# Performance work log

Measured on AMD Instinct MI355X. Metric: run time of the kernel, lower is better.

Reference implementation:

```python
import jax, jax.numpy as jnp
import numpy as np

B, N, C, H, D = 1, 4096, 256, 8, 64  # batch, seq, channels, heads, head_dim


def setup_inputs() -> dict:
    key = jax.random.key(0)
    ks = jax.random.split(key, 11)
    s = 0.02
    return {
        "q_x": jax.random.normal(ks[0], (B, N, C), jnp.float32),
        "k_x": jax.random.normal(ks[1], (B, N, C), jnp.float32),
        "v_x": jax.random.normal(ks[2], (B, N, C), jnp.float32),
        "bias": jax.random.normal(ks[3], (B, 1, N, N), jnp.float32),
        "wq": jax.random.normal(ks[4], (H * D, C), jnp.float32) * s,
        "wk": jax.random.normal(ks[5], (H * D, C), jnp.float32) * s,
        "wv": jax.random.normal(ks[6], (H * D, C), jnp.float32) * s,
        "wg": jax.random.normal(ks[7], (H * D, C), jnp.float32) * s,
        "bg": jnp.ones((H * D,), jnp.float32),  # gating bias init = 1
        "wo": jax.random.normal(ks[8], (C, H * D), jnp.float32) * s,
        "bo": jnp.zeros((C,), jnp.float32),
        "q_chunk_size": 256,
        "kv_chunk_size": 1024,
    }


def reference(q_x, k_x, v_x, bias, wq, wk, wv, wg, bg, wo, bo,
              q_chunk_size, kv_chunk_size):
    # The chunked Rabe-Staats loop computes exact softmax attention; the
    # chunk sizes are memory knobs only, so the reference computes the
    # mathematically identical full attention.
    q = (q_x @ wq.T).reshape(*q_x.shape[:-1], H, D) / jnp.sqrt(jnp.asarray(D, q_x.dtype))
    k = (k_x @ wk.T).reshape(*k_x.shape[:-1], H, D)
    v = (v_x @ wv.T).reshape(*v_x.shape[:-1], H, D)
    logits = jnp.einsum("bqhd,bkhd->bhqk", q, k) + bias  # [B,H,Q,K]
    p = jax.nn.softmax(logits, axis=-1)
    o = jnp.einsum("bkhd,bhqk->bqhd", v, p)  # [B,Q,H,D]
    g = jax.nn.sigmoid(q_x @ wg.T + bg).reshape(*q_x.shape[:-1], H, D)
    o = o * g
    o = o.reshape(*o.shape[:-2], H * D)
    return o @ wo.T + bo
```

## Files before the change

kernel.cpp:

```cpp
#include <hip/hip_runtime.h>
#include <stdint.h>

#define NN 4096
#define CC 256
#define HD 512
#define DD 64
#define KSPLIT 3

typedef __attribute__((ext_vector_type(8))) short short8;
typedef __attribute__((ext_vector_type(4))) float floatx4;

__device__ __forceinline__ unsigned short f2bf(float x) {
    union { float f; unsigned int u; } v; v.f = x;
    unsigned int u = v.u + 0x7fffu + ((v.u >> 16) & 1u);
    return (unsigned short)(u >> 16);
}
__device__ __forceinline__ float bf2f(unsigned short s) {
    union { unsigned int u; float f; } v; v.u = ((unsigned int)s) << 16;
    return v.f;
}

#if defined(__has_builtin) && __has_builtin(__builtin_amdgcn_cvt_pk_bf16_f32)
typedef __attribute__((ext_vector_type(2))) __bf16 bf16x2_t;
__device__ __forceinline__ unsigned int pack2bf(float a, float b) {
    union { bf16x2_t v; unsigned int u; } x;
    x.v = __builtin_amdgcn_cvt_pk_bf16_f32(a, b);
    return x.u;
}
#else
__device__ __forceinline__ unsigned int pack2bf(float a, float b) {
    return ((unsigned int)f2bf(b) << 16) | (unsigned int)f2bf(a);
}
#endif

#define GLOAD_LDS(gp, lp) __builtin_amdgcn_global_load_lds(                    \
    (__attribute__((address_space(1))) void*)(gp),                             \
    (__attribute__((address_space(3))) void*)(lp), 16, 0, 0)

__global__ __launch_bounds__(256) void prep_kernel(
    const float* __restrict__ qx, const float* __restrict__ kx,
    const float* __restrict__ vx,
    const float* __restrict__ wq, const float* __restrict__ wk,
    const float* __restrict__ wv, const float* __restrict__ wg,
    const float* __restrict__ wo,
    unsigned short* __restrict__ qxb, unsigned short* __restrict__ kxb,
    unsigned short* __restrict__ vxb, unsigned short* __restrict__ Wb,
    unsigned short* __restrict__ wob)
{
    const int z = blockIdx.y;
    const float* src; unsigned short* dst; int n; float s = 1.0f;
    switch (z) {
        case 0: src = qx; dst = qxb; n = NN * CC; break;
        case 1: src = kx; dst = kxb; n = NN * CC; break;
        case 2: src = vx; dst = vxb; n = NN * CC; break;
        case 3: src = wq; dst = Wb;               n = HD * CC; s = 0.125f; break;
        case 4: src = wk; dst = Wb + 1 * HD * CC; n = HD * CC; break;
        case 5: src = wv; dst = Wb + 2 * HD * CC; n = HD * CC; break;
        case 6: src = wg; dst = Wb + 3 * HD * CC; n = HD * CC; break;
        default: src = wo; dst = wob;             n = CC * HD; break;
    }
    int i = (blockIdx.x * 256 + threadIdx.x) * 4;
    if (i < n) {
        float4 v = *(const float4*)&src[i];
        ushort4 p;
        p.x = f2bf(v.x * s); p.y = f2bf(v.y * s);
        p.z = f2bf(v.z * s); p.w = f2bf(v.w * s);
        *(ushort4*)&dst[i] = p;
    }
}

__global__ __launch_bounds__(256, 4) void proj_kernel(
    const unsigned short* __restrict__ qxb, const unsigned short* __restrict__ kxb,
    const unsigned short* __restrict__ vxb, const unsigned short* __restrict__ Wb,
    const float* __restrict__ bg,
    unsigned short* __restrict__ Qb, unsigned short* __restrict__ Kb,
    unsigned short* __restrict__ VbT, unsigned short* __restrict__ Gb)
{
    const int m0 = blockIdx.x * 128;
    const int nb = blockIdx.y;
    const int n0 = nb * 128;
    const int mode = nb >> 2;
    const unsigned short* X = (mode == 1) ? kxb : (mode == 2) ? vxb : qxb;

    const int tid = threadIdx.x;
    const int wid = tid >> 6;
    const int wr = wid >> 1, wc = wid & 1;
    const int lane = tid & 63;
    const int quad = lane >> 4;
    const int ln = lane & 15;
    const int lnx = ln & 7;

    __shared__ __align__(16) unsigned short smem[128 * 136];
    unsigned short* Xs = smem;
    unsigned short* Ws = smem + 128 * 64;

    floatx4 acc[4][4] = {};

    for (int k0 = 0; k0 < CC; k0 += 64) {
        #pragma unroll
        for (int t = 0; t < 4; t++) {
            int row = wid * 32 + t * 8 + (lane >> 3);
            int c = (lane & 7) ^ (lane >> 3);
            GLOAD_LDS(&X[(size_t)(m0 + row) * CC + k0 + c * 8],
                      &Xs[(wid * 32 + t * 8) * 64]);
            GLOAD_LDS(&Wb[(size_t)(n0 + row) * CC + k0 + c * 8],
                      &Ws[(wid * 32 + t * 8) * 64]);
        }
        __syncthreads();

        #pragma unroll
        for (int ks = 0; ks < 64; ks += 32) {
            const int cb = ks >> 3;
            short8 a[4], b[4];
            #pragma unroll
            for (int i = 0; i < 4; i++)
                a[i] = *(const short8*)&Xs[(wr * 64 + i * 16 + ln) * 64 +
                                           (((quad ^ cb) ^ lnx) * 8)];
            #pragma unroll
            for (int j = 0; j < 4; j++)
                b[j] = *(const short8*)&Ws[(wc * 64 + j * 16 + ln) * 64 +
                                           (((quad ^ cb) ^ lnx) * 8)];
            #pragma unroll
            for (int i = 0; i < 4; i++)
                #pragma unroll
                for (int j = 0; j < 4; j++)
                    acc[i][j] = __builtin_amdgcn_mfma_f32_16x16x32_bf16(a[i], b[j], acc[i][j], 0, 0, 0);
        }
        __syncthreads();
    }

    const int subn = nb & 3;
    if (mode != 2) {
        unsigned short* Out = (mode == 0) ? Qb : (mode == 1) ? Kb : Gb;
        #pragma unroll
        for (int i = 0; i < 4; i++) {
            #pragma unroll
            for (int j = 0; j < 4; j++) {
                int col = subn * 128 + wc * 64 + j * 16 + ln;
                float bgv = (mode == 3) ? bg[col] : 0.0f;
                #pragma unroll
                for (int r = 0; r < 4; r++) {
                    int row = m0 + wr * 64 + i * 16 + quad * 4 + r;
                    float v = acc[i][j][r];
                    if (mode == 3) v = 1.0f / (1.0f + __expf(-(v + bgv)));
                    Out[(size_t)row * HD + col] = f2bf(v);
                }
            }
        }
    } else {
        #pragma unroll
        for (int i = 0; i < 4; i++) {
            #pragma unroll
            for (int j = 0; j < 4; j++) {
                int cl = wc * 64 + j * 16 + ln;
                #pragma unroll
                for (int r = 0; r < 4; r++) {
                    int rl = wr * 64 + i * 16 + quad * 4 + r;
                    smem[cl * 136 + rl] = f2bf(acc[i][j][r]);
                }
            }
        }
        __syncthreads();
        #pragma unroll
        for (int it = 0; it < 8; it++) {
            int idx = it * 256 + tid;
            int c = idx >> 4, ch = idx & 15;
            short8 vv = *(const short8*)&smem[c * 136 + ch * 8];
            *(short8*)&VbT[(size_t)(subn * 128 + c) * NN + m0 + ch * 8] = vv;
        }
    }
}

__global__ __launch_bounds__(256, 6) void attn_kernel(
    const unsigned short* __restrict__ Qb, const unsigned short* __restrict__ Kb,
    const unsigned short* __restrict__ VbT,
    const float* __restrict__ bias,
    unsigned short* __restrict__ Opart, float* __restrict__ Lpart)
{
    const int h = blockIdx.y;
    const int q0 = blockIdx.x * 64;
    const int sp = blockIdx.z;
    const int tbeg = (sp * 64) / KSPLIT;
    const int tend = ((sp + 1) * 64) / KSPLIT;
    const int tid = threadIdx.x;
    const int wid = tid >> 6;
    const int lane = tid & 63;
    const int quad = lane >> 4;
    const int ln = lane & 15;
    const int lnx = ln & 7;

    __shared__ __align__(16) unsigned short Ks[64 * 64];
    __shared__ __align__(16) unsigned short Vs[64 * 64];
    __shared__ __align__(16) unsigned short Ps[64 * 72];

    const int qrow = q0 + wid * 16 + ln;
    short8 qa0 = *(const short8*)&Qb[(size_t)qrow * HD + h * DD + quad * 8];
    short8 qa1 = *(const short8*)&Qb[(size_t)qrow * HD + h * DD + 32 + quad * 8];

    floatx4 O[4] = {};
    float lsum[4] = {0.0f, 0.0f, 0.0f, 0.0f};

    for (int kt = tbeg; kt < tend; kt++) {
        const int k0 = kt * 64;
        #pragma unroll
        for (int t = 0; t < 2; t++) {
            int row = wid * 16 + t * 8 + (lane >> 3);
            int c = (lane & 7) ^ (lane >> 3);
            GLOAD_LDS(&Kb[(size_t)(k0 + row) * HD + h * DD + c * 8],
                      &Ks[(wid * 16 + t * 8) * 64]);
            GLOAD_LDS(&VbT[(size_t)(h * DD + row) * NN + k0 + c * 8],
                      &Vs[(wid * 16 + t * 8) * 64]);
        }

        float bv[4][4];
        #pragma unroll
        for (int r = 0; r < 4; r++) {
            const float* brow = &bias[(size_t)(q0 + wid * 16 + quad * 4 + r) * NN + k0];
            #pragma unroll
            for (int n = 0; n < 4; n++) bv[r][n] = brow[n * 16 + ln];
        }
        __syncthreads();

        floatx4 S[4];
        #pragma unroll
        for (int n = 0; n < 4; n++)
            S[n] = (floatx4){bv[0][n], bv[1][n], bv[2][n], bv[3][n]};
        #pragma unroll
        for (int n = 0; n < 4; n++) {
            short8 b0 = *(const short8*)&Ks[(n * 16 + ln) * 64 + ((quad ^ lnx) * 8)];
            S[n] = __builtin_amdgcn_mfma_f32_16x16x32_bf16(qa0, b0, S[n], 0, 0, 0);
            short8 b1 = *(const short8*)&Ks[(n * 16 + ln) * 64 + (((quad ^ 4) ^ lnx) * 8)];
            S[n] = __builtin_amdgcn_mfma_f32_16x16x32_bf16(qa1, b1, S[n], 0, 0, 0);
        }

        #pragma unroll
        for (int r = 0; r < 4; r++) {
            int prow = (wid * 16 + quad * 4 + r) * 72;
            #pragma unroll
            for (int n = 0; n < 4; n += 2) {
                float p0 = __expf(S[n][r]);
                float p1 = __expf(S[n + 1][r]);
                lsum[r] += p0 + p1;
                unsigned int pk = pack2bf(p0, p1);
                Ps[prow + n * 16 + ln] = (unsigned short)(pk & 0xffffu);
                Ps[prow + (n + 1) * 16 + ln] = (unsigned short)(pk >> 16);
            }
        }

        #pragma unroll
        for (int ks = 0; ks < 64; ks += 32) {
            const int cb = ks >> 3;
            short8 a = *(const short8*)&Ps[(wid * 16 + ln) * 72 + ks + quad * 8];
            #pragma unroll
            for (int nd = 0; nd < 4; nd++) {
                short8 b = *(const short8*)&Vs[(nd * 16 + ln) * 64 +
                                               (((quad ^ cb) ^ lnx) * 8)];
                O[nd] = __builtin_amdgcn_mfma_f32_16x16x32_bf16(a, b, O[nd], 0, 0, 0);
            }
        }
        __syncthreads();
    }

    #pragma unroll
    for (int r = 0; r < 4; r++) {
        #pragma unroll
        for (int off = 1; off < 16; off <<= 1)
            lsum[r] += __shfl_xor(lsum[r], off);
        int grow = q0 + wid * 16 + quad * 4 + r;
        size_t base = ((size_t)(sp * 8 + h) * NN + grow) * 64;
        #pragma unroll
        for (int nd = 0; nd < 4; nd++)
            Opart[base + nd * 16 + ln] = f2bf(O[nd][r]);
        if (ln == 0)
            Lpart[(size_t)(sp * 8 + h) * NN + grow] = lsum[r];
    }
}

__global__ __launch_bounds__(256) void combine_kernel(
    const unsigned short* __restrict__ Opart, const float* __restrict__ Lpart,
    const unsigned short* __restrict__ Gb, unsigned short* __restrict__ OGb)
{
    const int tid = threadIdx.x;
    const int d = tid & 63;
    const int flat = blockIdx.x * 4 + (tid >> 6);
    const int h = flat >> 12;
    const int q = flat & (NN - 1);

    float l = 0.0f, o = 0.0f;
    #pragma unroll
    for (int sp = 0; sp < KSPLIT; sp++) {
        size_t idx = (size_t)(sp * 8 + h) * NN + q;
        l += Lpart[idx];
        o += bf2f(Opart[idx * 64 + d]);
    }
    float inv = 1.0f / l;
    int col = h * DD + d;
    float g = bf2f(Gb[(size_t)q * HD + col]);
    OGb[(size_t)q * HD + col] = f2bf(o * inv * g);
}

__global__ __launch_bounds__(256, 4) void outproj_kernel(
    const unsigned short* __restrict__ OGb, const unsigned short* __restrict__ wob,
    const float* __restrict__ bo, float* __restrict__ out)
{
    const int m0 = blockIdx.x * 64;
    const int n0 = blockIdx.y * 64;
    const int tid = threadIdx.x;
    const int wid = tid >> 6;
    const int lane = tid & 63;
    const int quad = lane >> 4;
    const int ln = lane & 15;
    const int lnx = ln & 7;

    __shared__ __align__(16) unsigned short Xs[64 * 64];
    __shared__ __align__(16) unsigned short Ws[64 * 64];

    floatx4 acc[4] = {};

    for (int k0 = 0; k0 < HD; k0 += 64) {
        #pragma unroll
        for (int t = 0; t < 2; t++) {
            int row = wid * 16 + t * 8 + (lane >> 3);
            int c = (lane & 7) ^ (lane >> 3);
            GLOAD_LDS(&OGb[(size_t)(m0 + row) * HD + k0 + c * 8],
                      &Xs[(wid * 16 + t * 8) * 64]);
            GLOAD_LDS(&wob[(size_t)(n0 + row) * HD + k0 + c * 8],
                      &Ws[(wid * 16 + t * 8) * 64]);
        }
        __syncthreads();

        #pragma unroll
        for (int ks = 0; ks < 64; ks += 32) {
            const int cb = ks >> 3;
            short8 a = *(const short8*)&Xs[(wid * 16 + ln) * 64 +
                                           (((quad ^ cb) ^ lnx) * 8)];
            #pragma unroll
            for (int n = 0; n < 4; n++) {
                short8 b = *(const short8*)&Ws[(n * 16 + ln) * 64 +
                                               (((quad ^ cb) ^ lnx) * 8)];
                acc[n] = __builtin_amdgcn_mfma_f32_16x16x32_bf16(a, b, acc[n], 0, 0, 0);
            }
        }
        __syncthreads();
    }

    #pragma unroll
    for (int n = 0; n < 4; n++) {
        int col = n0 + n * 16 + ln;
        float bov = bo[col];
        #pragma unroll
        for (int r = 0; r < 4; r++) {
            int row = m0 + wid * 16 + quad * 4 + r;
            out[(size_t)row * CC + col] = acc[n][r] + bov;
        }
    }
}

extern "C" void kernel_launch(void* const* d_in, const int* in_sizes, int n_in,
                              void* d_out, int out_size, void* d_ws, size_t ws_size,
                              hipStream_t stream) {
    const float* qx   = (const float*)d_in[0];
    const float* kx   = (const float*)d_in[1];
    const float* vx   = (const float*)d_in[2];
    const float* bias = (const float*)d_in[3];
    const float* wq   = (const float*)d_in[4];
    const float* wk   = (const float*)d_in[5];
    const float* wv   = (const float*)d_in[6];
    const float* wg   = (const float*)d_in[7];
    const float* bg   = (const float*)d_in[8];
    const float* wo   = (const float*)d_in[9];
    const float* bo   = (const float*)d_in[10];
    float* out = (float*)d_out;

    char* ws = (char*)d_ws;
    const size_t MB = (size_t)1 << 20;
    unsigned short* wob   = (unsigned short*)(ws);
    float*          Lpart = (float*)(ws + MB / 4);
    unsigned short* Qb    = (unsigned short*)(ws + 1 * MB);
    unsigned short* Kb    = (unsigned short*)(ws + 5 * MB);
    unsigned short* VbT   = (unsigned short*)(ws + 9 * MB);
    unsigned short* Gb    = (unsigned short*)(ws + 13 * MB);
    unsigned short* OGb   = (unsigned short*)(ws + 17 * MB);
    unsigned short* qxb   = (unsigned short*)(ws + 21 * MB);
    unsigned short* kxb   = (unsigned short*)(ws + 23 * MB);
    unsigned short* vxb   = (unsigned short*)(ws + 25 * MB);
    unsigned short* Wb    = (unsigned short*)(ws + 27 * MB);
    unsigned short* Opart = (unsigned short*)(ws + 21 * MB);

    prep_kernel<<<dim3(NN * CC / (256 * 4), 8), 256, 0, stream>>>(
        qx, kx, vx, wq, wk, wv, wg, wo, qxb, kxb, vxb, Wb, wob);
    proj_kernel<<<dim3(32, 16), 256, 0, stream>>>(
        qxb, kxb, vxb, Wb, bg, Qb, Kb, VbT, Gb);
    attn_kernel<<<dim3(64, 8, KSPLIT), 256, 0, stream>>>(
        Qb, Kb, VbT, bias, Opart, Lpart);
    combine_kernel<<<dim3(NN * 8 / 4), 256, 0, stream>>>(
        Opart, Lpart, Gb, OGb);
    outproj_kernel<<<dim3(64, 4), 256, 0, stream>>>(
        OGb, wob, bo, out);
}
```

Before: 213.6 us.

## Shrink projection tiles and split-K the output projection for more blocks

```diff
diff --git a/kernel.cpp b/kernel.cpp
--- a/kernel.cpp
+++ b/kernel.cpp
@@ -6,6 +6,7 @@
 #define HD 512
 #define DD 64
 #define KSPLIT 3
+#define KSPLIT_O 4
 
 typedef __attribute__((ext_vector_type(8))) short short8;
 typedef __attribute__((ext_vector_type(4))) float floatx4;
@@ -76,7 +77,7 @@
     unsigned short* __restrict__ Qb, unsigned short* __restrict__ Kb,
     unsigned short* __restrict__ VbT, unsigned short* __restrict__ Gb)
 {
-    const int m0 = blockIdx.x * 128;
+    const int m0 = blockIdx.x * 64;
     const int nb = blockIdx.y;
     const int n0 = nb * 128;
     const int mode = nb >> 2;
@@ -84,25 +85,29 @@
 
     const int tid = threadIdx.x;
     const int wid = tid >> 6;
-    const int wr = wid >> 1, wc = wid & 1;
     const int lane = tid & 63;
     const int quad = lane >> 4;
     const int ln = lane & 15;
     const int lnx = ln & 7;
 
-    __shared__ __align__(16) unsigned short smem[128 * 136];
+    __shared__ __align__(16) unsigned short smem[64 * 64 + 128 * 64];
     unsigned short* Xs = smem;
-    unsigned short* Ws = smem + 128 * 64;
-
-    floatx4 acc[4][4] = {};
+    unsigned short* Ws = smem + 64 * 64;
+
+    floatx4 acc[8] = {};
 
     for (int k0 = 0; k0 < CC; k0 += 64) {
+        #pragma unroll
+        for (int t = 0; t < 2; t++) {
+            int row = wid * 16 + t * 8 + (lane >> 3);
+            int c = (lane & 7) ^ (lane >> 3);
+            GLOAD_LDS(&X[(size_t)(m0 + row) * CC + k0 + c * 8],
+                      &Xs[(wid * 16 + t * 8) * 64]);
+        }
         #pragma unroll
         for (int t = 0; t < 4; t++) {
             int row = wid * 32 + t * 8 + (lane >> 3);
             int c = (lane & 7) ^ (lane >> 3);
-            GLOAD_LDS(&X[(size_t)(m0 + row) * CC + k0 + c * 8],
-                      &Xs[(wid * 32 + t * 8) * 64]);
             GLOAD_LDS(&Wb[(size_t)(n0 + row) * CC + k0 + c * 8],
                       &Ws[(wid * 32 + t * 8) * 64]);
         }
@@ -111,20 +116,14 @@
         #pragma unroll
         for (int ks = 0; ks < 64; ks += 32) {
             const int cb = ks >> 3;
-            short8 a[4], b[4];
-            #pragma unroll
-            for (int i = 0; i < 4; i++)
-                a[i] = *(const short8*)&Xs[(wr * 64 + i * 16 + ln) * 64 +
+            short8 a = *(const short8*)&Xs[(wid * 16 + ln) * 64 +
                                            (((quad ^ cb) ^ lnx) * 8)];
             #pragma unroll
-            for (int j = 0; j < 4; j++)
-                b[j] = *(const short8*)&Ws[(wc * 64 + j * 16 + ln) * 64 +
-                                           (((quad ^ cb) ^ lnx) * 8)];
-            #pragma unroll
-            for (int i = 0; i < 4; i++)
-                #pragma unroll
-                for (int j = 0; j < 4; j++)
-                    acc[i][j] = __builtin_amdgcn_mfma_f32_16x16x32_bf16(a[i], b[j], acc[i][j], 0, 0, 0);
+            for (int j = 0; j < 8; j++) {
+                short8 b = *(const short8*)&Ws[(j * 16 + ln) * 64 +
+                                               (((quad ^ cb) ^ lnx) * 8)];
+                acc[j] = __builtin_amdgcn_mfma_f32_16x16x32_bf16(a, b, acc[j], 0, 0, 0);
+            }
         }
         __syncthreads();
     }
@@ -133,39 +132,33 @@
     if (mode != 2) {
         unsigned short* Out = (mode == 0) ? Qb : (mode == 1) ? Kb : Gb;
         #pragma unroll
-        for (int i = 0; i < 4; i++) {
-            #pragma unroll
-            for (int j = 0; j < 4; j++) {
-                int col = subn * 128 + wc * 64 + j * 16 + ln;
-                float bgv = (mode == 3) ? bg[col] : 0.0f;
-                #pragma unroll
-                for (int r = 0; r < 4; r++) {
-                    int row = m0 + wr * 64 + i * 16 + quad * 4 + r;
-                    float v = acc[i][j][r];
-                    if (mode == 3) v = 1.0f / (1.0f + __expf(-(v + bgv)));
-                    Out[(size_t)row * HD + col] = f2bf(v);
-                }
+        for (int j = 0; j < 8; j++) {
+            int col = subn * 128 + j * 16 + ln;
+            float bgv = (mode == 3) ? bg[col] : 0.0f;
+            #pragma unroll
+            for (int r = 0; r < 4; r++) {
+                int row = m0 + wid * 16 + quad * 4 + r;
+                float v = acc[j][r];
+                if (mode == 3) v = 1.0f / (1.0f + __expf(-(v + bgv)));
+                Out[(size_t)row * HD + col] = f2bf(v);
             }
         }
     } else {
         #pragma unroll
-        for (int i = 0; i < 4; i++) {
-            #pragma unroll
-            for (int j = 0; j < 4; j++) {
-                int cl = wc * 64 + j * 16 + ln;
-                #pragma unroll
-                for (int r = 0; r < 4; r++) {
-                    int rl = wr * 64 + i * 16 + quad * 4 + r;
-                    smem[cl * 136 + rl] = f2bf(acc[i][j][r]);
-                }
-            }
-        }
-        __syncthreads();
-        #pragma unroll
-        for (int it = 0; it < 8; it++) {
+        for (int j = 0; j < 8; j++) {
+            int cl = j * 16 + ln;
+            #pragma unroll
+            for (int r = 0; r < 4; r++) {
+                int rl = wid * 16 + quad * 4 + r;
+                smem[cl * 72 + rl] = f2bf(acc[j][r]);
+            }
+        }
+        __syncthreads();
+        #pragma unroll
+        for (int it = 0; it < 4; it++) {
             int idx = it * 256 + tid;
-            int c = idx >> 4, ch = idx & 15;
-            short8 vv = *(const short8*)&smem[c * 136 + ch * 8];
+            int c = idx >> 3, ch = idx & 7;
+            short8 vv = *(const short8*)&smem[c * 72 + ch * 8];
             *(short8*)&VbT[(size_t)(subn * 128 + c) * NN + m0 + ch * 8] = vv;
         }
     }
@@ -301,10 +294,11 @@
 
 __global__ __launch_bounds__(256, 4) void outproj_kernel(
     const unsigned short* __restrict__ OGb, const unsigned short* __restrict__ wob,
-    const float* __restrict__ bo, float* __restrict__ out)
+    float* __restrict__ Psum)
 {
     const int m0 = blockIdx.x * 64;
     const int n0 = blockIdx.y * 64;
+    const int sp = blockIdx.z;
     const int tid = threadIdx.x;
     const int wid = tid >> 6;
     const int lane = tid & 63;
@@ -317,7 +311,8 @@
 
     floatx4 acc[4] = {};
 
-    for (int k0 = 0; k0 < HD; k0 += 64) {
+    const int kbeg = sp * (HD / KSPLIT_O);
+    for (int k0 = kbeg; k0 < kbeg + HD / KSPLIT_O; k0 += 64) {
         #pragma unroll
         for (int t = 0; t < 2; t++) {
             int row = wid * 16 + t * 8 + (lane >> 3);
@@ -344,16 +339,33 @@
         __syncthreads();
     }
 
+    float* P = Psum + (size_t)sp * NN * CC;
     #pragma unroll
     for (int n = 0; n < 4; n++) {
         int col = n0 + n * 16 + ln;
-        float bov = bo[col];
         #pragma unroll
         for (int r = 0; r < 4; r++) {
             int row = m0 + wid * 16 + quad * 4 + r;
-            out[(size_t)row * CC + col] = acc[n][r] + bov;
-        }
-    }
+            P[(size_t)row * CC + col] = acc[n][r];
+        }
+    }
+}
+
+__global__ __launch_bounds__(256) void outfinal_kernel(
+    const float* __restrict__ Psum, const float* __restrict__ bo,
+    float* __restrict__ out)
+{
+    int i = (blockIdx.x * 256 + threadIdx.x) * 4;
+    float4 s = *(const float4*)&Psum[i];
+    #pragma unroll
+    for (int sp = 1; sp < KSPLIT_O; sp++) {
+        float4 p = *(const float4*)&Psum[(size_t)sp * NN * CC + i];
+        s.x += p.x; s.y += p.y; s.z += p.z; s.w += p.w;
+    }
+    int col = i & (CC - 1);
+    float4 b = *(const float4*)&bo[col];
+    s.x += b.x; s.y += b.y; s.z += b.z; s.w += b.w;
+    *(float4*)&out[i] = s;
 }
 
 extern "C" void kernel_launch(void* const* d_in, const int* in_sizes, int n_in,
@@ -386,15 +398,18 @@
     unsigned short* vxb   = (unsigned short*)(ws + 25 * MB);
     unsigned short* Wb    = (unsigned short*)(ws + 27 * MB);
     unsigned short* Opart = (unsigned short*)(ws + 21 * MB);
+    float*          Psum  = (float*)(ws + 21 * MB);
 
     prep_kernel<<<dim3(NN * CC / (256 * 4), 8), 256, 0, stream>>>(
         qx, kx, vx, wq, wk, wv, wg, wo, qxb, kxb, vxb, Wb, wob);
-    proj_kernel<<<dim3(32, 16), 256, 0, stream>>>(
+    proj_kernel<<<dim3(64, 16), 256, 0, stream>>>(
         qxb, kxb, vxb, Wb, bg, Qb, Kb, VbT, Gb);
     attn_kernel<<<dim3(64, 8, KSPLIT), 256, 0, stream>>>(
         Qb, Kb, VbT, bias, Opart, Lpart);
     combine_kernel<<<dim3(NN * 8 / 4), 256, 0, stream>>>(
         Opart, Lpart, Gb, OGb);
-    outproj_kernel<<<dim3(64, 4), 256, 0, stream>>>(
-        OGb, wob, bo, out);
-}
+    outproj_kernel<<<dim3(64, 4, KSPLIT_O), 256, 0, stream>>>(
+        OGb, wob, Psum);
+    outfinal_kernel<<<dim3(NN * CC / (256 * 4)), 256, 0, stream>>>(
+        Psum, bo, out);
+}
```

Measured after the change: 220.0 us. 1.03x slower.
